# Kernel optimization log

Measured on AMD Instinct MI355X. Metric: run time of the kernel, lower is better.

Reference implementation:

```python
import jax, jax.numpy as jnp
import numpy as np

HEAD_SIZE = 64
HEADS = 12

def _rope(x):
    # x: [B, L, d]; bert4torch interleaved RoPE: q*cos + rotate_every_two(q)*sin
    L, d = x.shape[-2], x.shape[-1]
    inv_freq = 1.0 / (10000.0 ** (jnp.arange(0, d, 2, dtype=jnp.float32) / d))
    ang = jnp.arange(L, dtype=jnp.float32)[:, None] * inv_freq  # [L, d/2]
    sin = jnp.repeat(jnp.sin(ang), 2, axis=-1)  # [L, d]
    cos = jnp.repeat(jnp.cos(ang), 2, axis=-1)  # [L, d]
    x2 = jnp.stack([-x[..., 1::2], x[..., ::2]], axis=-1).reshape(x.shape)
    return x * cos + x2 * sin

def setup_inputs() -> dict:
    key = jax.random.key(0)
    ks = jax.random.split(key, 4)
    B, L, H = 2, 2048, 1024
    inputs = jax.random.normal(ks[0], (B, L, H), dtype=jnp.float32)
    mask = jnp.ones((B, L), dtype=jnp.int32)
    Wp = jax.random.normal(ks[1], (H, 2 * HEAD_SIZE), dtype=jnp.float32) * (1.0 / np.sqrt(H))
    bp = jnp.zeros((2 * HEAD_SIZE,), dtype=jnp.float32)
    Wq = jax.random.normal(ks[2], (2 * HEAD_SIZE, 2 * HEADS), dtype=jnp.float32) * (1.0 / np.sqrt(2 * HEAD_SIZE))
    bq = jnp.zeros((2 * HEADS,), dtype=jnp.float32)
    return {"inputs": inputs, "mask": mask, "Wp": Wp, "bp": bp, "Wq": Wq, "bq": bq}

def reference(inputs, mask, Wp, bp, Wq, bq):
    B, L, _ = inputs.shape
    seq_out = inputs @ Wp + bp                          # [B, L, 2*hs]
    qw, kw = seq_out[..., :HEAD_SIZE], seq_out[..., HEAD_SIZE:]
    qw, kw = _rope(qw), _rope(kw)
    scores = jnp.einsum('bmd,bnd->bmn', qw, kw) / jnp.sqrt(jnp.float32(HEAD_SIZE))  # [B, L, L]
    # chunk(heads, -1) + stack(-2) == reshape(B, L, heads, 2); transpose(1,2) -> [B, H, L, 2]
    bias = (seq_out @ Wq + bq).reshape(B, L, HEADS, 2) / 2.0
    bias = jnp.transpose(bias, (0, 2, 1, 3))            # [B, H, L, 2]
    logits = scores[:, None] + bias[..., :1] + jnp.swapaxes(bias[..., 1:], 2, 3)  # [B, H, L, L]
    m = mask.astype(bool)
    neg_inf = jnp.float32(-jnp.inf)
    logits = jnp.where(m[:, None, :, None], logits, neg_inf)
    logits = jnp.where(m[:, None, None, :], logits, neg_inf)
    tril = jnp.tril(jnp.ones((L, L), dtype=logits.dtype), -1)
    logits = logits - tril * jnp.float32(1e12)
    return logits
```

## Files before the change

### kernel.cpp

```cpp
#include <hip/hip_runtime.h>
#include <math.h>

#define LSEQ 2048
#define NB 2
#define HDIM 1024
#define NKV 128
#define MALL (NB*LSEQ)
#define KSPLIT 4

__global__ __launch_bounds__(256) void k1_gemm(const float* __restrict__ A,
                                               const float* __restrict__ Wp,
                                               float* __restrict__ Cp) {
    const int nt    = blockIdx.x & 1;
    const int split = blockIdx.x >> 1;
    const int m0 = blockIdx.y * 64;
    const int n0 = nt * 64;
    __shared__ float As[32][68];
    __shared__ float Bs[32][64];
    const int tid = threadIdx.x;
    const int tm = tid & 15;
    const int tn = tid >> 4;
    float acc[4][4] = {};
    for (int kc = 0; kc < 8; ++kc) {
        const int k0 = split*256 + kc*32;
        #pragma unroll
        for (int p = 0; p < 2; ++p) {
            int idx = tid + 256*p;
            int row = idx >> 3, kq = idx & 7;
            float4 a = *(const float4*)(A + (size_t)(m0+row)*HDIM + k0 + 4*kq);
            As[4*kq+0][row] = a.x;
            As[4*kq+1][row] = a.y;
            As[4*kq+2][row] = a.z;
            As[4*kq+3][row] = a.w;
        }
        #pragma unroll
        for (int p = 0; p < 2; ++p) {
            int idx = tid + 256*p;
            int r = idx >> 4, c = idx & 15;
            *(float4*)(&Bs[r][4*c]) = *(const float4*)(Wp + (size_t)(k0+r)*NKV + n0 + 4*c);
        }
        __syncthreads();
        #pragma unroll
        for (int kk = 0; kk < 32; ++kk) {
            float4 av = *(const float4*)(&As[kk][4*tm]);
            float4 bv = *(const float4*)(&Bs[kk][4*tn]);
            float aa[4] = {av.x, av.y, av.z, av.w};
            float bb[4] = {bv.x, bv.y, bv.z, bv.w};
            #pragma unroll
            for (int i = 0; i < 4; ++i)
                #pragma unroll
                for (int j = 0; j < 4; ++j)
                    acc[i][j] = fmaf(aa[i], bb[j], acc[i][j]);
        }
        __syncthreads();
    }
    float* outp = Cp + (size_t)split*MALL*NKV;
    #pragma unroll
    for (int i = 0; i < 4; ++i) {
        float4 v = make_float4(acc[i][0], acc[i][1], acc[i][2], acc[i][3]);
        *(float4*)(outp + (size_t)(m0 + 4*tm + i)*NKV + n0 + 4*tn) = v;
    }
}

__global__ __launch_bounds__(64) void k2_rope_bias(const float* __restrict__ Cp,
        const float* __restrict__ bp, const float* __restrict__ Wq,
        const float* __restrict__ bq, float* __restrict__ qwout,
        float* __restrict__ kwout, float* __restrict__ biasQ,
        float* __restrict__ biasK) {
    const int row = blockIdx.x;
    const int b = row >> 11;
    const int l = row & (LSEQ - 1);
    const int t = threadIdx.x;
    float x0 = bp[2*t], x1 = bp[2*t+1];
    #pragma unroll
    for (int s = 0; s < KSPLIT; ++s) {
        const float* r = Cp + (size_t)s*MALL*NKV + (size_t)row*NKV;
        x0 += r[2*t];
        x1 += r[2*t+1];
    }
    const int p = t & 31;
    float inv = exp2f(-0.41524101186098287f * (float)p);
    float ang = (float)l * inv;
    float sn = sinf(ang), cs = cosf(ang);
    float y0 = x0*cs - x1*sn;
    float y1 = x1*cs + x0*sn;
    float* dst = (t < 32) ? (qwout + (size_t)row*64) : (kwout + (size_t)row*64);
    dst[2*p]   = y0;
    dst[2*p+1] = y1;
    float res = 0.f;
    for (int j = 0; j < 24; ++j) {
        float part = fmaf(x0, Wq[(2*t)*24 + j], x1 * Wq[(2*t+1)*24 + j]);
        #pragma unroll
        for (int off = 32; off > 0; off >>= 1)
            part += __shfl_xor(part, off);
        if (t == j) res = part;
    }
    if (t < 24) {
        float v = (res + bq[t]) * 0.5f;
        int h = t >> 1;
        float* bb = (t & 1) ? biasK : biasQ;
        bb[((size_t)b*12 + h)*LSEQ + l] = v;
    }
}

__global__ __launch_bounds__(512, 2) void k3_scores(const float* __restrict__ qw,
        const float* __restrict__ kwv, const float* __restrict__ biasQ,
        const float* __restrict__ biasK, const int* __restrict__ mask,
        float* __restrict__ out) {
    extern __shared__ float kws[];
    const int m0  = blockIdx.x * 8;
    const int b   = blockIdx.y;
    const int tid = threadIdx.x;
    const int w   = tid >> 6;
    const int l   = tid & 63;
    const size_t rowbase = (size_t)b * LSEQ;
    const int m = m0 + w;
    const int swz = l & 7;

    float4 q4[16];
    {
        const float4* qp = (const float4*)(qw + (rowbase + m)*64);
        #pragma unroll
        for (int j = 0; j < 16; ++j) q4[j] = qp[j];
    }
    float bqh[12];
    #pragma unroll
    for (int h = 0; h < 12; ++h) bqh[h] = biasQ[((size_t)b*12 + h)*LSEQ + m];
    const bool okm = mask[rowbase + m] != 0;
    const size_t outrow = (size_t)b*12*LSEQ*LSEQ + (size_t)m*LSEQ;

    #pragma unroll
    for (int p = 0; p < 8; ++p) {
        int F = tid + 512*p;
        int r = F >> 4, qd = F & 15;
        float4 v = *(const float4*)(kwv + (rowbase + r)*64 + 4*qd);
        *(float4*)(&kws[r*64 + 4*(qd ^ ((r>>2)&7))]) = v;
    }
    asm volatile("s_waitcnt lgkmcnt(0)" ::: "memory");
    __builtin_amdgcn_s_barrier();
    asm volatile("" ::: "memory");

    for (int s = 0; s < 8; ++s) {
        const int cur = (s & 1) * 16384;
        const int nxt = ((s + 1) & 1) * 16384;
        const bool more = (s + 1) < 8;

        float4 pre[8];
        if (more) {
            const int n1 = (s + 1) * 256;
            #pragma unroll
            for (int p = 0; p < 8; ++p) {
                int F = tid + 512*p;
                int r = F >> 4, qd = F & 15;
                pre[p] = *(const float4*)(kwv + (rowbase + n1 + r)*64 + 4*qd);
            }
        }

        float acc0 = 0.f, acc1 = 0.f, acc2 = 0.f, acc3 = 0.f;
        const float* kb = kws + cur + 256*l;
        #pragma unroll
        for (int j = 0; j < 16; ++j) {
            const int qo = 4*(j ^ swz);
            float4 k0 = *(const float4*)(kb + qo);
            float4 k1 = *(const float4*)(kb + 64 + qo);
            float4 k2 = *(const float4*)(kb + 128 + qo);
            float4 k3 = *(const float4*)(kb + 192 + qo);
            float4 qv = q4[j];
            acc0 = fmaf(qv.x,k0.x,fmaf(qv.y,k0.y,fmaf(qv.z,k0.z,fmaf(qv.w,k0.w,acc0))));
            acc1 = fmaf(qv.x,k1.x,fmaf(qv.y,k1.y,fmaf(qv.z,k1.z,fmaf(qv.w,k1.w,acc1))));
            acc2 = fmaf(qv.x,k2.x,fmaf(qv.y,k2.y,fmaf(qv.z,k2.z,fmaf(qv.w,k2.w,acc2))));
            acc3 = fmaf(qv.x,k3.x,fmaf(qv.y,k3.y,fmaf(qv.z,k3.z,fmaf(qv.w,k3.w,acc3))));
        }

        const int nq = s*256 + 4*l;
        int4 mq = *(const int4*)(mask + rowbase + nq);
        float t0 = (okm && mq.x) ? fmaf(acc0, 0.125f, (m > nq+0) ? -1e12f : 0.f) : -INFINITY;
        float t1 = (okm && mq.y) ? fmaf(acc1, 0.125f, (m > nq+1) ? -1e12f : 0.f) : -INFINITY;
        float t2 = (okm && mq.z) ? fmaf(acc2, 0.125f, (m > nq+2) ? -1e12f : 0.f) : -INFINITY;
        float t3 = (okm && mq.w) ? fmaf(acc3, 0.125f, (m > nq+3) ? -1e12f : 0.f) : -INFINITY;
        const float* bkbase = biasK + (size_t)b*12*LSEQ + nq;
        float* op = out + outrow + nq;
        #pragma unroll
        for (int h = 0; h < 12; ++h) {
            float4 bk = *(const float4*)(bkbase + (size_t)h*LSEQ);
            float bq = bqh[h];
            float4 v;
            v.x = t0 + bq + bk.x;
            v.y = t1 + bq + bk.y;
            v.z = t2 + bq + bk.z;
            v.w = t3 + bq + bk.w;
            *(float4*)(op + (size_t)h*LSEQ*LSEQ) = v;
        }

        if (more) {
            #pragma unroll
            for (int p = 0; p < 8; ++p) {
                int F = tid + 512*p;
                int r = F >> 4, qd = F & 15;
                *(float4*)(&kws[nxt + r*64 + 4*(qd ^ ((r>>2)&7))]) = pre[p];
            }
            asm volatile("s_waitcnt lgkmcnt(0)" ::: "memory");
            __builtin_amdgcn_s_barrier();
            asm volatile("" ::: "memory");
        }
    }
}

extern "C" void kernel_launch(void* const* d_in, const int* in_sizes, int n_in,
                              void* d_out, int out_size, void* d_ws, size_t ws_size,
                              hipStream_t stream) {
    const float* inputs = (const float*)d_in[0];
    const int*   mask   = (const int*)  d_in[1];
    const float* Wp     = (const float*)d_in[2];
    const float* bp     = (const float*)d_in[3];
    const float* Wq     = (const float*)d_in[4];
    const float* bq     = (const float*)d_in[5];
    float* out = (float*)d_out;

    float* Cp  = (float*)d_ws;
    float* qwb = Cp  + (size_t)KSPLIT*MALL*NKV;
    float* kwb = qwb + (size_t)MALL*64;
    float* bQ  = kwb + (size_t)MALL*64;
    float* bK  = bQ  + (size_t)NB*12*LSEQ;

    k1_gemm     <<<dim3(8, 64),   256, 0, stream>>>(inputs, Wp, Cp);
    k2_rope_bias<<<dim3(MALL),     64, 0, stream>>>(Cp, bp, Wq, bq, qwb, kwb, bQ, bK);
    k3_scores   <<<dim3(256, 2), 512, 131072, stream>>>(qwb, kwb, bQ, bK, mask, out);
}
```

Measured before the change: 521.8 us.

## Split score computation from per-head bias fanout into separate kernels

The scores kernel now only computes the raw scaled QK^T into head 0's output slot, with two query rows per wave and no double-buffered K prefetch. A new fanout kernel reads those scores and writes all 12 heads with bias, mask and causal penalty using nontemporal stores, doing head 0 last in a separate pass so it can overwrite in place. The aim is to decouple the write-bound fanout from the compute loop. The cost is an extra write and re-read of a full L×L scores buffer per batch, plus one more kernel launch.

```diff
diff --git a/kernel.cpp b/kernel.cpp
--- a/kernel.cpp
+++ b/kernel.cpp
@@ -7,6 +7,8 @@
 #define NKV 128
 #define MALL (NB*LSEQ)
 #define KSPLIT 4
+
+typedef float vf4 __attribute__((ext_vector_type(4)));
 
 __global__ __launch_bounds__(256) void k1_gemm(const float* __restrict__ A,
                                                const float* __restrict__ Wp,
@@ -103,61 +105,41 @@
     }
 }
 
-__global__ __launch_bounds__(512, 2) void k3_scores(const float* __restrict__ qw,
-        const float* __restrict__ kwv, const float* __restrict__ biasQ,
-        const float* __restrict__ biasK, const int* __restrict__ mask,
-        float* __restrict__ out) {
+__global__ __launch_bounds__(256, 2) void k3_scores(const float* __restrict__ qw,
+        const float* __restrict__ kwv, float* __restrict__ out) {
     extern __shared__ float kws[];
     const int m0  = blockIdx.x * 8;
     const int b   = blockIdx.y;
     const int tid = threadIdx.x;
     const int w   = tid >> 6;
     const int l   = tid & 63;
+    const int swz = l & 7;
     const size_t rowbase = (size_t)b * LSEQ;
-    const int m = m0 + w;
-    const int swz = l & 7;
-
-    float4 q4[16];
+    const int mA = m0 + 2*w, mB = mA + 1;
+
+    float4 qa[16], qb[16];
     {
-        const float4* qp = (const float4*)(qw + (rowbase + m)*64);
-        #pragma unroll
-        for (int j = 0; j < 16; ++j) q4[j] = qp[j];
-    }
-    float bqh[12];
-    #pragma unroll
-    for (int h = 0; h < 12; ++h) bqh[h] = biasQ[((size_t)b*12 + h)*LSEQ + m];
-    const bool okm = mask[rowbase + m] != 0;
-    const size_t outrow = (size_t)b*12*LSEQ*LSEQ + (size_t)m*LSEQ;
-
-    #pragma unroll
-    for (int p = 0; p < 8; ++p) {
-        int F = tid + 512*p;
-        int r = F >> 4, qd = F & 15;
-        float4 v = *(const float4*)(kwv + (rowbase + r)*64 + 4*qd);
-        *(float4*)(&kws[r*64 + 4*(qd ^ ((r>>2)&7))]) = v;
-    }
-    asm volatile("s_waitcnt lgkmcnt(0)" ::: "memory");
-    __builtin_amdgcn_s_barrier();
-    asm volatile("" ::: "memory");
+        const float4* pa = (const float4*)(qw + (rowbase + mA)*64);
+        const float4* pb = (const float4*)(qw + (rowbase + mB)*64);
+        #pragma unroll
+        for (int j = 0; j < 16; ++j) { qa[j] = pa[j]; qb[j] = pb[j]; }
+    }
+    float* S = out + (size_t)b*12*LSEQ*LSEQ;
 
     for (int s = 0; s < 8; ++s) {
-        const int cur = (s & 1) * 16384;
-        const int nxt = ((s + 1) & 1) * 16384;
-        const bool more = (s + 1) < 8;
-
-        float4 pre[8];
-        if (more) {
-            const int n1 = (s + 1) * 256;
-            #pragma unroll
-            for (int p = 0; p < 8; ++p) {
-                int F = tid + 512*p;
-                int r = F >> 4, qd = F & 15;
-                pre[p] = *(const float4*)(kwv + (rowbase + n1 + r)*64 + 4*qd);
-            }
-        }
-
-        float acc0 = 0.f, acc1 = 0.f, acc2 = 0.f, acc3 = 0.f;
-        const float* kb = kws + cur + 256*l;
+        __syncthreads();
+        #pragma unroll
+        for (int p = 0; p < 16; ++p) {
+            int F = tid + 256*p;
+            int r = F >> 4, qd = F & 15;
+            float4 v = *(const float4*)(kwv + (rowbase + s*256 + r)*64 + 4*qd);
+            *(float4*)(&kws[r*64 + 4*(qd ^ ((r>>2)&7))]) = v;
+        }
+        __syncthreads();
+
+        float a0=0.f,a1=0.f,a2=0.f,a3=0.f;
+        float c0=0.f,c1=0.f,c2=0.f,c3=0.f;
+        const float* kb = kws + 256*l;
         #pragma unroll
         for (int j = 0; j < 16; ++j) {
             const int qo = 4*(j ^ swz);
@@ -165,44 +147,64 @@
             float4 k1 = *(const float4*)(kb + 64 + qo);
             float4 k2 = *(const float4*)(kb + 128 + qo);
             float4 k3 = *(const float4*)(kb + 192 + qo);
-            float4 qv = q4[j];
-            acc0 = fmaf(qv.x,k0.x,fmaf(qv.y,k0.y,fmaf(qv.z,k0.z,fmaf(qv.w,k0.w,acc0))));
-            acc1 = fmaf(qv.x,k1.x,fmaf(qv.y,k1.y,fmaf(qv.z,k1.z,fmaf(qv.w,k1.w,acc1))));
-            acc2 = fmaf(qv.x,k2.x,fmaf(qv.y,k2.y,fmaf(qv.z,k2.z,fmaf(qv.w,k2.w,acc2))));
-            acc3 = fmaf(qv.x,k3.x,fmaf(qv.y,k3.y,fmaf(qv.z,k3.z,fmaf(qv.w,k3.w,acc3))));
-        }
-
+            float4 qv = qa[j];
+            a0 = fmaf(qv.x,k0.x,fmaf(qv.y,k0.y,fmaf(qv.z,k0.z,fmaf(qv.w,k0.w,a0))));
+            a1 = fmaf(qv.x,k1.x,fmaf(qv.y,k1.y,fmaf(qv.z,k1.z,fmaf(qv.w,k1.w,a1))));
+            a2 = fmaf(qv.x,k2.x,fmaf(qv.y,k2.y,fmaf(qv.z,k2.z,fmaf(qv.w,k2.w,a2))));
+            a3 = fmaf(qv.x,k3.x,fmaf(qv.y,k3.y,fmaf(qv.z,k3.z,fmaf(qv.w,k3.w,a3))));
+            qv = qb[j];
+            c0 = fmaf(qv.x,k0.x,fmaf(qv.y,k0.y,fmaf(qv.z,k0.z,fmaf(qv.w,k0.w,c0))));
+            c1 = fmaf(qv.x,k1.x,fmaf(qv.y,k1.y,fmaf(qv.z,k1.z,fmaf(qv.w,k1.w,c1))));
+            c2 = fmaf(qv.x,k2.x,fmaf(qv.y,k2.y,fmaf(qv.z,k2.z,fmaf(qv.w,k2.w,c2))));
+            c3 = fmaf(qv.x,k3.x,fmaf(qv.y,k3.y,fmaf(qv.z,k3.z,fmaf(qv.w,k3.w,c3))));
+        }
         const int nq = s*256 + 4*l;
-        int4 mq = *(const int4*)(mask + rowbase + nq);
-        float t0 = (okm && mq.x) ? fmaf(acc0, 0.125f, (m > nq+0) ? -1e12f : 0.f) : -INFINITY;
-        float t1 = (okm && mq.y) ? fmaf(acc1, 0.125f, (m > nq+1) ? -1e12f : 0.f) : -INFINITY;
-        float t2 = (okm && mq.z) ? fmaf(acc2, 0.125f, (m > nq+2) ? -1e12f : 0.f) : -INFINITY;
-        float t3 = (okm && mq.w) ? fmaf(acc3, 0.125f, (m > nq+3) ? -1e12f : 0.f) : -INFINITY;
-        const float* bkbase = biasK + (size_t)b*12*LSEQ + nq;
-        float* op = out + outrow + nq;
-        #pragma unroll
-        for (int h = 0; h < 12; ++h) {
-            float4 bk = *(const float4*)(bkbase + (size_t)h*LSEQ);
-            float bq = bqh[h];
-            float4 v;
-            v.x = t0 + bq + bk.x;
-            v.y = t1 + bq + bk.y;
-            v.z = t2 + bq + bk.z;
-            v.w = t3 + bq + bk.w;
-            *(float4*)(op + (size_t)h*LSEQ*LSEQ) = v;
-        }
-
-        if (more) {
-            #pragma unroll
-            for (int p = 0; p < 8; ++p) {
-                int F = tid + 512*p;
-                int r = F >> 4, qd = F & 15;
-                *(float4*)(&kws[nxt + r*64 + 4*(qd ^ ((r>>2)&7))]) = pre[p];
-            }
-            asm volatile("s_waitcnt lgkmcnt(0)" ::: "memory");
-            __builtin_amdgcn_s_barrier();
-            asm volatile("" ::: "memory");
-        }
+        float4 va = make_float4(a0*0.125f, a1*0.125f, a2*0.125f, a3*0.125f);
+        float4 vb = make_float4(c0*0.125f, c1*0.125f, c2*0.125f, c3*0.125f);
+        *(float4*)(S + (size_t)mA*LSEQ + nq) = va;
+        *(float4*)(S + (size_t)mB*LSEQ + nq) = vb;
+    }
+}
+
+__global__ __launch_bounds__(256) void k4_fanout(const float* __restrict__ biasQ,
+        const float* __restrict__ biasK, const int* __restrict__ mask,
+        float* __restrict__ out, int pass) {
+    int b, h;
+    if (pass == 0) { b = blockIdx.y / 11; h = 1 + blockIdx.y % 11; }
+    else           { b = blockIdx.y;      h = 0; }
+    const int m0  = blockIdx.x * 16;
+    const int tid = threadIdx.x;
+    const size_t rowb = (size_t)b * LSEQ;
+    const float* S = out + (size_t)b*12*LSEQ*LSEQ;
+    float* O = out + ((size_t)b*12 + h)*LSEQ*LSEQ;
+    const int nA = 4*tid, nB = 4*tid + 1024;
+
+    const float* bkp = biasK + ((size_t)b*12 + h)*LSEQ;
+    const float4 bkA = *(const float4*)(bkp + nA);
+    const float4 bkB = *(const float4*)(bkp + nB);
+    const int4 mnA = *(const int4*)(mask + rowb + nA);
+    const int4 mnB = *(const int4*)(mask + rowb + nB);
+    const float* bqp = biasQ + ((size_t)b*12 + h)*LSEQ;
+
+    #pragma unroll 4
+    for (int r = 0; r < 16; ++r) {
+        const int m = m0 + r;
+        const float bq = bqp[m];
+        const bool okm = mask[rowb + m] != 0;
+        const float* srow = S + (size_t)m*LSEQ;
+        float4 sA = *(const float4*)(srow + nA);
+        float4 sB = *(const float4*)(srow + nB);
+        vf4 vA, vB;
+        vA.x = (okm && mnA.x) ? (sA.x + bq + bkA.x) - ((m > nA+0) ? 1e12f : 0.f) : -INFINITY;
+        vA.y = (okm && mnA.y) ? (sA.y + bq + bkA.y) - ((m > nA+1) ? 1e12f : 0.f) : -INFINITY;
+        vA.z = (okm && mnA.z) ? (sA.z + bq + bkA.z) - ((m > nA+2) ? 1e12f : 0.f) : -INFINITY;
+        vA.w = (okm && mnA.w) ? (sA.w + bq + bkA.w) - ((m > nA+3) ? 1e12f : 0.f) : -INFINITY;
+        vB.x = (okm && mnB.x) ? (sB.x + bq + bkB.x) - ((m > nB+0) ? 1e12f : 0.f) : -INFINITY;
+        vB.y = (okm && mnB.y) ? (sB.y + bq + bkB.y) - ((m > nB+1) ? 1e12f : 0.f) : -INFINITY;
+        vB.z = (okm && mnB.z) ? (sB.z + bq + bkB.z) - ((m > nB+2) ? 1e12f : 0.f) : -INFINITY;
+        vB.w = (okm && mnB.w) ? (sB.w + bq + bkB.w) - ((m > nB+3) ? 1e12f : 0.f) : -INFINITY;
+        __builtin_nontemporal_store(vA, (vf4*)(O + (size_t)m*LSEQ + nA));
+        __builtin_nontemporal_store(vB, (vf4*)(O + (size_t)m*LSEQ + nB));
     }
 }
 
@@ -225,5 +227,7 @@
 
     k1_gemm     <<<dim3(8, 64),   256, 0, stream>>>(inputs, Wp, Cp);
     k2_rope_bias<<<dim3(MALL),     64, 0, stream>>>(Cp, bp, Wq, bq, qwb, kwb, bQ, bK);
-    k3_scores   <<<dim3(256, 2), 512, 131072, stream>>>(qwb, kwb, bQ, bK, mask, out);
-}
+    k3_scores   <<<dim3(256, 2), 256, 65536, stream>>>(qwb, kwb, out);
+    k4_fanout   <<<dim3(128, 22), 256, 0, stream>>>(bQ, bK, mask, out, 0);
+    k4_fanout   <<<dim3(128, 2),  256, 0, stream>>>(bQ, bK, mask, out, 1);
+}
```

Result: slower. 588.9 us (+12.9%).

## Restructure score kernel: 256-thread blocks, 128-key chunks, nontemporal output stores

Applied to the files above, without the earlier changes.

The scores kernel now runs 256-thread blocks, with half a wave (32 lanes) per query row. It walks the keys in 16 double-buffered chunks of 128 instead of 8 chunks of 256, which halves the LDS footprint to 64 KB, and widens the XOR swizzle to 16 slots. The biasK vectors and the mask are loaded before the epilogue behind a sched_barrier, and the 12 per-head outputs are written with nontemporal stores. The goal is to cut cache pollution from the large write-only output and to raise occupancy and overlap. In exchange there are more barriers, shorter contiguous write runs per row, and inline asm without memory clobbers.

```diff
diff --git a/kernel.cpp b/kernel.cpp
--- a/kernel.cpp
+++ b/kernel.cpp
@@ -7,6 +7,8 @@
 #define NKV 128
 #define MALL (NB*LSEQ)
 #define KSPLIT 4
+
+typedef float vf4 __attribute__((ext_vector_type(4)));
 
 __global__ __launch_bounds__(256) void k1_gemm(const float* __restrict__ A,
                                                const float* __restrict__ Wp,
@@ -103,7 +105,7 @@
     }
 }
 
-__global__ __launch_bounds__(512, 2) void k3_scores(const float* __restrict__ qw,
+__global__ __launch_bounds__(256, 2) void k3_scores(const float* __restrict__ qw,
         const float* __restrict__ kwv, const float* __restrict__ biasQ,
         const float* __restrict__ biasK, const int* __restrict__ mask,
         float* __restrict__ out) {
@@ -111,11 +113,10 @@
     const int m0  = blockIdx.x * 8;
     const int b   = blockIdx.y;
     const int tid = threadIdx.x;
-    const int w   = tid >> 6;
-    const int l   = tid & 63;
+    const int l5  = tid & 31;
+    const int m   = m0 + (tid >> 5);
+    const int key = l5 & 15;
     const size_t rowbase = (size_t)b * LSEQ;
-    const int m = m0 + w;
-    const int swz = l & 7;
 
     float4 q4[16];
     {
@@ -127,81 +128,86 @@
     #pragma unroll
     for (int h = 0; h < 12; ++h) bqh[h] = biasQ[((size_t)b*12 + h)*LSEQ + m];
     const bool okm = mask[rowbase + m] != 0;
-    const size_t outrow = (size_t)b*12*LSEQ*LSEQ + (size_t)m*LSEQ;
 
     #pragma unroll
     for (int p = 0; p < 8; ++p) {
-        int F = tid + 512*p;
-        int r = F >> 4, qd = F & 15;
-        float4 v = *(const float4*)(kwv + (rowbase + r)*64 + 4*qd);
-        *(float4*)(&kws[r*64 + 4*(qd ^ ((r>>2)&7))]) = v;
-    }
-    asm volatile("s_waitcnt lgkmcnt(0)" ::: "memory");
+        int F = tid + 256*p;
+        int r = F >> 4, q16 = F & 15;
+        float4 v = *(const float4*)(kwv + (rowbase + r)*64 + 4*q16);
+        *(float4*)(&kws[r*64 + 4*(q16 ^ ((r>>2)&15))]) = v;
+    }
+    asm volatile("s_waitcnt lgkmcnt(0)");
     __builtin_amdgcn_s_barrier();
-    asm volatile("" ::: "memory");
-
-    for (int s = 0; s < 8; ++s) {
-        const int cur = (s & 1) * 16384;
-        const int nxt = ((s + 1) & 1) * 16384;
-        const bool more = (s + 1) < 8;
+
+    for (int c = 0; c < 16; ++c) {
+        const int nb  = c * 128;
+        const int cur = (c & 1) * 8192;
+        const int n0  = nb + 4*l5;
+
+        float4 a = {0.f, 0.f, 0.f, 0.f};
+        const float* rb = kws + cur + 4*l5*64;
+        #pragma unroll
+        for (int j = 0; j < 16; ++j) {
+            const int col = 4*(j ^ key);
+            float4 k0 = *(const float4*)(rb + col);
+            float4 k1 = *(const float4*)(rb + 64  + col);
+            float4 k2 = *(const float4*)(rb + 128 + col);
+            float4 k3 = *(const float4*)(rb + 192 + col);
+            float4 qv = q4[j];
+            a.x = fmaf(qv.x,k0.x,fmaf(qv.y,k0.y,fmaf(qv.z,k0.z,fmaf(qv.w,k0.w,a.x))));
+            a.y = fmaf(qv.x,k1.x,fmaf(qv.y,k1.y,fmaf(qv.z,k1.z,fmaf(qv.w,k1.w,a.y))));
+            a.z = fmaf(qv.x,k2.x,fmaf(qv.y,k2.y,fmaf(qv.z,k2.z,fmaf(qv.w,k2.w,a.z))));
+            a.w = fmaf(qv.x,k3.x,fmaf(qv.y,k3.y,fmaf(qv.z,k3.z,fmaf(qv.w,k3.w,a.w))));
+        }
+        a.x *= 0.125f; a.y *= 0.125f; a.z *= 0.125f; a.w *= 0.125f;
 
         float4 pre[8];
-        if (more) {
-            const int n1 = (s + 1) * 256;
+        if (c < 15) {
             #pragma unroll
             for (int p = 0; p < 8; ++p) {
-                int F = tid + 512*p;
-                int r = F >> 4, qd = F & 15;
-                pre[p] = *(const float4*)(kwv + (rowbase + n1 + r)*64 + 4*qd);
+                int F = tid + 256*p;
+                int r = F >> 4, q16 = F & 15;
+                pre[p] = *(const float4*)(kwv + (rowbase + nb + 128 + r)*64 + 4*q16);
             }
         }
-
-        float acc0 = 0.f, acc1 = 0.f, acc2 = 0.f, acc3 = 0.f;
-        const float* kb = kws + cur + 256*l;
-        #pragma unroll
-        for (int j = 0; j < 16; ++j) {
-            const int qo = 4*(j ^ swz);
-            float4 k0 = *(const float4*)(kb + qo);
-            float4 k1 = *(const float4*)(kb + 64 + qo);
-            float4 k2 = *(const float4*)(kb + 128 + qo);
-            float4 k3 = *(const float4*)(kb + 192 + qo);
-            float4 qv = q4[j];
-            acc0 = fmaf(qv.x,k0.x,fmaf(qv.y,k0.y,fmaf(qv.z,k0.z,fmaf(qv.w,k0.w,acc0))));
-            acc1 = fmaf(qv.x,k1.x,fmaf(qv.y,k1.y,fmaf(qv.z,k1.z,fmaf(qv.w,k1.w,acc1))));
-            acc2 = fmaf(qv.x,k2.x,fmaf(qv.y,k2.y,fmaf(qv.z,k2.z,fmaf(qv.w,k2.w,acc2))));
-            acc3 = fmaf(qv.x,k3.x,fmaf(qv.y,k3.y,fmaf(qv.z,k3.z,fmaf(qv.w,k3.w,acc3))));
-        }
-
-        const int nq = s*256 + 4*l;
-        int4 mq = *(const int4*)(mask + rowbase + nq);
-        float t0 = (okm && mq.x) ? fmaf(acc0, 0.125f, (m > nq+0) ? -1e12f : 0.f) : -INFINITY;
-        float t1 = (okm && mq.y) ? fmaf(acc1, 0.125f, (m > nq+1) ? -1e12f : 0.f) : -INFINITY;
-        float t2 = (okm && mq.z) ? fmaf(acc2, 0.125f, (m > nq+2) ? -1e12f : 0.f) : -INFINITY;
-        float t3 = (okm && mq.w) ? fmaf(acc3, 0.125f, (m > nq+3) ? -1e12f : 0.f) : -INFINITY;
-        const float* bkbase = biasK + (size_t)b*12*LSEQ + nq;
-        float* op = out + outrow + nq;
+        float4 bkv[12];
+        #pragma unroll
+        for (int h = 0; h < 12; ++h)
+            bkv[h] = *(const float4*)(biasK + ((size_t)b*12 + h)*LSEQ + n0);
+        const int4 mq = *(const int4*)(mask + rowbase + n0);
+        __builtin_amdgcn_sched_barrier(0);
+
+        const bool ok0 = okm && (mq.x != 0);
+        const bool ok1 = okm && (mq.y != 0);
+        const bool ok2 = okm && (mq.z != 0);
+        const bool ok3 = okm && (mq.w != 0);
+        const float p0 = (m > n0+0) ? 1e12f : 0.f;
+        const float p1 = (m > n0+1) ? 1e12f : 0.f;
+        const float p2 = (m > n0+2) ? 1e12f : 0.f;
+        const float p3 = (m > n0+3) ? 1e12f : 0.f;
+        float* op = out + ((size_t)b*12*LSEQ + (size_t)m)*LSEQ + n0;
         #pragma unroll
         for (int h = 0; h < 12; ++h) {
-            float4 bk = *(const float4*)(bkbase + (size_t)h*LSEQ);
-            float bq = bqh[h];
-            float4 v;
-            v.x = t0 + bq + bk.x;
-            v.y = t1 + bq + bk.y;
-            v.z = t2 + bq + bk.z;
-            v.w = t3 + bq + bk.w;
-            *(float4*)(op + (size_t)h*LSEQ*LSEQ) = v;
-        }
-
-        if (more) {
+            const float4 bk = bkv[h];
+            const float bqv = bqh[h];
+            vf4 v;
+            v.x = (ok0 ? (a.x + bqv + bk.x) : -INFINITY) - p0;
+            v.y = (ok1 ? (a.y + bqv + bk.y) : -INFINITY) - p1;
+            v.z = (ok2 ? (a.z + bqv + bk.z) : -INFINITY) - p2;
+            v.w = (ok3 ? (a.w + bqv + bk.w) : -INFINITY) - p3;
+            __builtin_nontemporal_store(v, (vf4*)(op + (size_t)h*LSEQ*LSEQ));
+        }
+
+        if (c < 15) {
+            const int nxt = ((c + 1) & 1) * 8192;
             #pragma unroll
             for (int p = 0; p < 8; ++p) {
-                int F = tid + 512*p;
-                int r = F >> 4, qd = F & 15;
-                *(float4*)(&kws[nxt + r*64 + 4*(qd ^ ((r>>2)&7))]) = pre[p];
+                int F = tid + 256*p;
+                int r = F >> 4, q16 = F & 15;
+                *(float4*)(&kws[nxt + r*64 + 4*(q16 ^ ((r>>2)&15))]) = pre[p];
             }
-            asm volatile("s_waitcnt lgkmcnt(0)" ::: "memory");
+            asm volatile("s_waitcnt lgkmcnt(0)");
             __builtin_amdgcn_s_barrier();
-            asm volatile("" ::: "memory");
         }
     }
 }
@@ -225,5 +231,5 @@
 
     k1_gemm     <<<dim3(8, 64),   256, 0, stream>>>(inputs, Wp, Cp);
     k2_rope_bias<<<dim3(MALL),     64, 0, stream>>>(Cp, bp, Wq, bq, qwb, kwb, bQ, bK);
-    k3_scores   <<<dim3(256, 2), 512, 131072, stream>>>(qwb, kwb, bQ, bK, mask, out);
-}
+    k3_scores   <<<dim3(256, 2), 256, 65536, stream>>>(qwb, kwb, bQ, bK, mask, out);
+}
```

Result: faster. 491.2 us (-5.9%).
